# Optimization experiments

Measured on AMD Instinct MI355X. Metric: run time of the kernel, lower is better.

The kernel has to match this reference:

```python
import jax, jax.numpy as jnp
import numpy as np
import math

BS, S, DIM, H = 2, 2048, 1024, 16
DH = DIM // H


def setup_inputs() -> dict:
    key = jax.random.key(0)
    ks = jax.random.split(key, 11)
    std = 1.0 / math.sqrt(DIM)
    inp = {
        "query": jax.random.normal(ks[0], (BS, S, DIM), jnp.float32),
        "key_": jax.random.normal(ks[1], (BS, S, DIM), jnp.float32),
        "value": jax.random.normal(ks[2], (BS, S, DIM), jnp.float32),
        "mask": jnp.ones((BS, S), jnp.int32),
        "q_w": jax.random.normal(ks[3], (DIM, DIM), jnp.float32) * std,
        "q_b": jnp.zeros((DIM,), jnp.float32),
        "k_w": jax.random.normal(ks[4], (DIM, DIM), jnp.float32) * std,
        "k_b": jnp.zeros((DIM,), jnp.float32),
        "v_w": jax.random.normal(ks[5], (DIM, DIM), jnp.float32) * std,
        "v_b": jnp.zeros((DIM,), jnp.float32),
        "o_w": jax.random.normal(ks[6], (DIM, DIM), jnp.float32) * std,
        "o_b": jnp.zeros((DIM,), jnp.float32),
    }
    return inp


def _shape(x):
    # (bs, s, dim) -> (bs, h, s, dh)
    return x.reshape(BS, -1, H, DH).transpose(0, 2, 1, 3)


def reference(query, key_, value, mask, q_w, q_b, k_w, k_b, v_w, v_b, o_w, o_b):
    # linear projections (torch Linear: x @ W.T + b)
    q = _shape(query @ q_w.T + q_b) / math.sqrt(DH)
    k = _shape(key_ @ k_w.T + k_b)
    v = _shape(value @ v_w.T + v_b)
    # scores: (bs, h, s, s)
    scores = jnp.einsum("bhqd,bhkd->bhqk", q, k)
    pad = (mask == 0)[:, None, None, :]  # (bs,1,1,k_len)
    scores = jnp.where(pad, -jnp.inf, scores)
    weights = jax.nn.softmax(scores, axis=-1)
    context = jnp.einsum("bhqk,bhkd->bhqd", weights, v)
    context = context.transpose(0, 2, 1, 3).reshape(BS, -1, DIM)
    return context @ o_w.T + o_b
```

## Files before the change

### kernel.cpp

```cpp
#include <hip/hip_runtime.h>
#include <hip/hip_bf16.h>

#define BSZ 2
#define SEQ 2048
#define DIMN 1024
#define NH 16
#define DH 64
#define LOG2E 1.4426950408889634f

typedef unsigned short ushort_t;
typedef __attribute__((ext_vector_type(8))) short short8;
typedef __attribute__((ext_vector_type(4))) float float4v;

__device__ __forceinline__ ushort_t f2bf(float f) {
    union { float f; unsigned int u; } c; c.f = f;
    return (ushort_t)((c.u + 0x8000u) >> 16);
}
__device__ __forceinline__ unsigned int pkbf(float a, float b) {
    __hip_bfloat162 h = __float22bfloat162_rn(make_float2(a, b));
    unsigned int u; __builtin_memcpy(&u, &h, 4); return u;
}
__device__ __forceinline__ unsigned int pkbf_asm(float a, float b) {
    unsigned int d;
    asm("v_cvt_pk_bf16_f32 %0, %1, %2" : "=v"(d) : "v"(a), "v"(b));
    return d;
}
__device__ __forceinline__ float exp2_raw(float x) {
    float d; asm("v_exp_f32 %0, %1" : "=v"(d) : "v"(x)); return d;
}
__device__ __forceinline__ float max3f(float a, float b, float c) {
    float d; asm("v_max3_f32 %0, %1, %2, %3" : "=v"(d) : "v"(a), "v"(b), "v"(c)); return d;
}
__device__ __forceinline__ void gld16(const ushort_t* g, ushort_t* l) {
    __builtin_amdgcn_global_load_lds(
        (const __attribute__((address_space(1))) unsigned int*)g,
        (__attribute__((address_space(3))) unsigned int*)l, 16, 0, 0);
}

__global__ __launch_bounds__(256) void cvt_w4(
    const float* __restrict__ w0, const float* __restrict__ w1,
    const float* __restrict__ w2, const float* __restrict__ w3,
    ushort_t* __restrict__ o0, ushort_t* __restrict__ o1,
    ushort_t* __restrict__ o2, ushort_t* __restrict__ o3)
{
    const float* s; ushort_t* d;
    switch (blockIdx.y) {
        case 0: s = w0; d = o0; break;
        case 1: s = w1; d = o1; break;
        case 2: s = w2; d = o2; break;
        default: s = w3; d = o3; break;
    }
    int i = (blockIdx.x * 256 + threadIdx.x) * 4;
    float4v v = *(const float4v*)(s + i);
    uint2 o; o.x = pkbf(v[0], v[1]); o.y = pkbf(v[2], v[3]);
    *(uint2*)(d + i) = o;
}

__global__ __launch_bounds__(256) void gemm_qkv_hyb(
    const float* __restrict__ xq, const float* __restrict__ xk, const float* __restrict__ xv,
    const ushort_t* __restrict__ Wq, const ushort_t* __restrict__ Wk, const ushort_t* __restrict__ Wv,
    const float* __restrict__ qb, const float* __restrict__ kb, const float* __restrict__ vb,
    ushort_t* __restrict__ Qp, ushort_t* __restrict__ Kp, ushort_t* __restrict__ VpT)
{
    __shared__ __align__(16) ushort_t As[128 * 64];
    __shared__ __align__(16) ushort_t Bs[128 * 64];
    const int tid  = threadIdx.x;
    const int lane = tid & 63;
    const int w    = tid >> 6;
    const int wm   = w >> 1, wn = w & 1;
    const int quad = lane >> 4;
    const int l16  = lane & 15;
    const int sw   = l16 & 7;

    const int orig = blockIdx.x;
    const int swz  = (orig & 7) * 96 + (orig >> 3);
    const int bx   = swz % 24;
    const int by   = swz / 24;

    const int mBase = by * 128;
    const int nGlob = bx * 128;
    const int z     = nGlob >> 10;
    const int nBase = nGlob & 1023;
    const float*    A    = (z == 0) ? xq : (z == 1) ? xk : xv;
    const ushort_t* W    = (z == 0) ? Wq : (z == 1) ? Wk : Wv;
    const float*    bias = (z == 0) ? qb : (z == 1) ? kb : vb;

    const int srow = tid >> 3;
    const int sc   = tid & 7;

    float4v acc[4][4];
    const float4v z4 = {0.f, 0.f, 0.f, 0.f};
#pragma unroll
    for (int i = 0; i < 4; ++i)
#pragma unroll
        for (int j = 0; j < 4; ++j) acc[i][j] = z4;

    for (int k0 = 0; k0 < 1024; k0 += 64) {
#pragma unroll
        for (int itq = 0; itq < 4; ++itq) {
            int row = itq * 32 + srow;
            int colsw = (sc ^ (row & 7)) * 8;
            gld16(W + (size_t)(nBase + row) * 1024 + k0 + colsw, &Bs[(itq * 32 + w * 8) * 64]);
        }
#pragma unroll
        for (int it = 0; it < 4; ++it) {
            int c = it * 256 + tid, row = c >> 3, col8 = c & 7;
            const float* g = A + (size_t)(mBase + row) * 1024 + k0 + col8 * 8;
            float4v a0 = *(const float4v*)g;
            float4v a1 = *(const float4v*)(g + 4);
            uint4 ua;
            ua.x = pkbf(a0[0], a0[1]); ua.y = pkbf(a0[2], a0[3]);
            ua.z = pkbf(a1[0], a1[1]); ua.w = pkbf(a1[2], a1[3]);
            *(uint4*)&As[row * 64 + ((col8 ^ (row & 7)) * 8)] = ua;
        }
        __syncthreads();

#pragma unroll
        for (int ksub = 0; ksub < 2; ++ksub) {
            short8 af[4], bf[4];
#pragma unroll
            for (int mt = 0; mt < 4; ++mt)
                af[mt] = *(const short8*)&As[(wm * 64 + mt * 16 + l16) * 64 + ((ksub * 4 + quad) ^ sw) * 8];
#pragma unroll
            for (int nt = 0; nt < 4; ++nt)
                bf[nt] = *(const short8*)&Bs[(wn * 64 + nt * 16 + l16) * 64 + ((ksub * 4 + quad) ^ sw) * 8];
#pragma unroll
            for (int mt = 0; mt < 4; ++mt)
#pragma unroll
                for (int nt = 0; nt < 4; ++nt)
                    acc[mt][nt] = __builtin_amdgcn_mfma_f32_16x16x32_bf16(af[mt], bf[nt], acc[mt][nt], 0, 0, 0);
        }
        __syncthreads();
    }

    const float scale = (z == 0) ? 0.125f * LOG2E : 1.0f;
    if (z < 2) {
        ushort_t* C = (z == 0) ? Qp : Kp;
#pragma unroll
        for (int mt = 0; mt < 4; ++mt)
#pragma unroll
            for (int nt = 0; nt < 4; ++nt) {
                int colg = nBase + wn * 64 + nt * 16 + l16;
                float bv = bias[colg];
#pragma unroll
                for (int r = 0; r < 4; ++r) {
                    int rowg = mBase + wm * 64 + mt * 16 + quad * 4 + r;
                    C[(size_t)rowg * 1024 + colg] = f2bf((acc[mt][nt][r] + bv) * scale);
                }
            }
    } else {
#pragma unroll
        for (int mt = 0; mt < 4; ++mt)
#pragma unroll
            for (int nt = 0; nt < 4; ++nt) {
                int n = nBase + wn * 64 + nt * 16 + l16;
                int hh = n >> 6, d = n & 63;
                float bv = bias[n];
                int rowg = mBase + wm * 64 + mt * 16 + quad * 4;
                int b = rowg >> 11, s = rowg & 2047;
                uint2 pk;
                pk.x = pkbf(acc[mt][nt][0] + bv, acc[mt][nt][1] + bv);
                pk.y = pkbf(acc[mt][nt][2] + bv, acc[mt][nt][3] + bv);
                *(uint2*)&VpT[(((size_t)(b * 16 + hh) * 64 + d) << 11) + s] = pk;
            }
    }
}

__global__ __launch_bounds__(256) void gemm_o(
    const ushort_t* __restrict__ A, const ushort_t* __restrict__ W,
    const float* __restrict__ bias, float* __restrict__ C)
{
    __shared__ __align__(16) ushort_t As[128 * 64];
    __shared__ __align__(16) ushort_t Bs[64 * 64];
    const int tid  = threadIdx.x;
    const int lane = tid & 63;
    const int w    = tid >> 6;
    const int wm   = w & 1, wn = w >> 1;
    const int quad = lane >> 4;
    const int l16  = lane & 15;
    const int sw   = l16 & 7;

    const int orig = blockIdx.x;
    const int swz  = (orig & 7) * 64 + (orig >> 3);
    const int nBase = (swz & 15) * 64;
    const int mBase = (swz >> 4) * 128;

    const int srow = tid >> 3;
    const int sc   = tid & 7;

    float4v acc[4][2];
    const float4v z4 = {0.f, 0.f, 0.f, 0.f};
#pragma unroll
    for (int mt = 0; mt < 4; ++mt)
#pragma unroll
        for (int nt = 0; nt < 2; ++nt) acc[mt][nt] = z4;

    for (int k0 = 0; k0 < 1024; k0 += 64) {
#pragma unroll
        for (int itq = 0; itq < 4; ++itq) {
            int row = itq * 32 + srow;
            gld16(A + (size_t)(mBase + row) * 1024 + k0 + ((sc ^ (row & 7)) * 8),
                  &As[(itq * 32 + w * 8) * 64]);
        }
#pragma unroll
        for (int itq = 0; itq < 2; ++itq) {
            int row = itq * 32 + srow;
            gld16(W + (size_t)(nBase + row) * 1024 + k0 + ((sc ^ (row & 7)) * 8),
                  &Bs[(itq * 32 + w * 8) * 64]);
        }
        __syncthreads();

#pragma unroll
        for (int ksub = 0; ksub < 2; ++ksub) {
            short8 af[4], bf[2];
#pragma unroll
            for (int mt = 0; mt < 4; ++mt)
                af[mt] = *(const short8*)&As[(wm * 64 + mt * 16 + l16) * 64 + ((ksub * 4 + quad) ^ sw) * 8];
#pragma unroll
            for (int nt = 0; nt < 2; ++nt)
                bf[nt] = *(const short8*)&Bs[(wn * 32 + nt * 16 + l16) * 64 + ((ksub * 4 + quad) ^ sw) * 8];
#pragma unroll
            for (int mt = 0; mt < 4; ++mt)
#pragma unroll
                for (int nt = 0; nt < 2; ++nt)
                    acc[mt][nt] = __builtin_amdgcn_mfma_f32_16x16x32_bf16(af[mt], bf[nt], acc[mt][nt], 0, 0, 0);
        }
        __syncthreads();
    }

#pragma unroll
    for (int mt = 0; mt < 4; ++mt)
#pragma unroll
        for (int nt = 0; nt < 2; ++nt) {
            int colg = nBase + wn * 32 + nt * 16 + l16;
            float bv = bias[colg];
#pragma unroll
            for (int r = 0; r < 4; ++r) {
                int rowg = mBase + wm * 64 + mt * 16 + quad * 4 + r;
                C[(size_t)rowg * 1024 + colg] = acc[mt][nt][r] + bv;
            }
        }
}

__global__ __launch_bounds__(512) void attn_kernel(
    const ushort_t* __restrict__ Qp, const ushort_t* __restrict__ Kp,
    const ushort_t* __restrict__ VpT, const int* __restrict__ mask,
    ushort_t* __restrict__ Cp)
{
    __shared__ __align__(16) ushort_t Ps[2][128 * 64];
    __shared__ __align__(16) ushort_t Ks[2][64 * 64];
    __shared__ __align__(16) ushort_t Vt[3][64 * 64];
    __shared__ int s_mok[8];

    const int tid  = threadIdx.x;
    const int lane = tid & 63;
    const int w    = tid >> 6;
    const int quad = lane >> 4;
    const int l16  = lane & 15;
    const int sw   = l16 & 7;
    const int b    = blockIdx.x >> 4;
    const int h    = blockIdx.x & 15;
    const int q0   = blockIdx.y * 128;

    const int srow = tid >> 3;
    const int sc   = tid & 7;
    const int gsc  = (sc ^ (srow & 7)) * 8;
    const ushort_t* Vbase = VpT + ((size_t)(b * 16 + h) * 64) * 2048;
    const ushort_t* Kbase = Kp + (size_t)b * SEQ * DIMN + h * DH;
    const ushort_t* Qbase = Qp + (size_t)(b * SEQ + q0) * DIMN + h * DH;

    {
        int m0 = mask[b * SEQ + tid];
        int m1 = mask[b * SEQ + 512 + tid];
        int m2 = mask[b * SEQ + 1024 + tid];
        int m3 = mask[b * SEQ + 1536 + tid];
        int ok = __all((m0 != 0) & (m1 != 0) & (m2 != 0) & (m3 != 0));
        if (lane == 0) s_mok[w] = ok;
    }

#pragma unroll
    for (int it2 = 0; it2 < 2; ++it2) {
        int row = it2 * 64 + srow;
        gld16(Qbase + (size_t)row * DIMN + ((sc ^ (row & 7)) * 8),
              &Ps[0][(it2 * 64 + w * 8) * 64]);
    }
    gld16(Kbase + (size_t)srow * DIMN + gsc, &Ks[0][w * 512]);
    gld16(Vbase + (size_t)srow * 2048 + gsc, &Vt[0][w * 512]);
    __syncthreads();

    const int mall = s_mok[0] & s_mok[1] & s_mok[2] & s_mok[3]
                   & s_mok[4] & s_mok[5] & s_mok[6] & s_mok[7];

    short8 bq[2];
#pragma unroll
    for (int ks = 0; ks < 2; ++ks)
        bq[ks] = *(const short8*)&Ps[0][(w * 16 + l16) * 64 + ((4 * ks + quad) ^ sw) * 8];

    const float4v z4 = {0.f, 0.f, 0.f, 0.f};
    float4v Oacc[4];
#pragma unroll
    for (int vt = 0; vt < 4; ++vt) Oacc[vt] = z4;
    float4v Lacc = z4;
    float mrow = 0.0f;
    float4v mneg4 = z4;

    short8 ones;
#pragma unroll
    for (int j = 0; j < 8; ++j) ones[j] = (short)0x3F80;

    const int NT = SEQ / 64;
    const int prow = (w * 16 + l16) * 64;

    {
        gld16(Kbase + (size_t)(64 + srow) * DIMN + gsc, &Ks[1][w * 512]);
        gld16(Vbase + (size_t)srow * 2048 + 64 + gsc, &Vt[1][w * 512]);

        float4v Sv[4];
        __builtin_amdgcn_s_setprio(1);
#pragma unroll
        for (int kt = 0; kt < 4; ++kt) {
            short8 ak = *(const short8*)&Ks[0][(kt * 16 + l16) * 64 + (quad ^ sw) * 8];
            Sv[kt] = __builtin_amdgcn_mfma_f32_16x16x32_bf16(ak, bq[0], mneg4, 0, 0, 0);
        }
#pragma unroll
        for (int kt = 0; kt < 4; ++kt) {
            short8 ak = *(const short8*)&Ks[0][(kt * 16 + l16) * 64 + ((4 + quad) ^ sw) * 8];
            Sv[kt] = __builtin_amdgcn_mfma_f32_16x16x32_bf16(ak, bq[1], Sv[kt], 0, 0, 0);
        }
        __builtin_amdgcn_s_setprio(0);

        if (!mall) {
#pragma unroll
            for (int kt = 0; kt < 4; ++kt) {
                int4 mv = *(const int4*)(mask + b * SEQ + kt * 16 + quad * 4);
#pragma unroll
                for (int r = 0; r < 4; ++r) {
                    int m = (r == 0) ? mv.x : (r == 1) ? mv.y : (r == 2) ? mv.z : mv.w;
                    Sv[kt][r] += (m == 0) ? -1e30f : 0.0f;
                }
            }
        }

        float a0 = max3f(Sv[0][0], Sv[0][1], Sv[0][2]);
        float a1 = max3f(Sv[0][3], Sv[1][0], Sv[1][1]);
        float a2 = max3f(Sv[1][2], Sv[1][3], Sv[2][0]);
        float a3 = max3f(Sv[2][1], Sv[2][2], Sv[2][3]);
        float a4 = max3f(Sv[3][0], Sv[3][1], Sv[3][2]);
        float b0 = max3f(a0, a1, Sv[3][3]);
        float b1 = max3f(a2, a3, a4);
        float mx = fmaxf(b0, b1);
        mx = fmaxf(mx, __shfl_xor(mx, 16));
        mx = fmaxf(mx, __shfl_xor(mx, 32));
        if (!__all(mx <= 8.0f)) {
            float d = fmaxf(mx, 0.0f);
            float alpha = exp2_raw(-d);
            mrow += d;
#pragma unroll
            for (int vt = 0; vt < 4; ++vt) Oacc[vt] *= alpha;
            Lacc *= alpha;
#pragma unroll
            for (int kt = 0; kt < 4; ++kt)
#pragma unroll
                for (int r = 0; r < 4; ++r) Sv[kt][r] -= d;
            mneg4[0] = -mrow; mneg4[1] = -mrow; mneg4[2] = -mrow; mneg4[3] = -mrow;
        }
#pragma unroll
        for (int kt = 0; kt < 4; ++kt)
#pragma unroll
            for (int r = 0; r < 4; ++r) Sv[kt][r] = exp2_raw(Sv[kt][r]);

#pragma unroll
        for (int kt = 0; kt < 4; ++kt) {
            uint2 pk;
            pk.x = pkbf_asm(Sv[kt][0], Sv[kt][1]);
            pk.y = pkbf_asm(Sv[kt][2], Sv[kt][3]);
            int chunk = (2 * kt + (quad >> 1)) ^ sw;
            *(uint2*)&Ps[0][prow + chunk * 8 + (quad & 1) * 4] = pk;
        }
        __syncthreads();
    }

    ushort_t* vRd  = Vt[0];
    ushort_t* vCur = Vt[1];
    ushort_t* vWr  = Vt[2];

#pragma unroll 2
    for (int t = 1; t < NT; ++t) {
        const int kt0 = t * 64;

        if (t + 1 < NT) {
            gld16(Kbase + (size_t)(kt0 + 64 + srow) * DIMN + gsc, &Ks[(t + 1) & 1][w * 512]);
            gld16(Vbase + (size_t)srow * 2048 + kt0 + 64 + gsc, vWr + w * 512);
        }

        float4v Sv[4];
        __builtin_amdgcn_s_setprio(1);
#pragma unroll
        for (int kt = 0; kt < 4; ++kt) {
            short8 ak = *(const short8*)&Ks[t & 1][(kt * 16 + l16) * 64 + (quad ^ sw) * 8];
            Sv[kt] = __builtin_amdgcn_mfma_f32_16x16x32_bf16(ak, bq[0], mneg4, 0, 0, 0);
        }
#pragma unroll
        for (int kt = 0; kt < 4; ++kt) {
            short8 ak = *(const short8*)&Ks[t & 1][(kt * 16 + l16) * 64 + ((4 + quad) ^ sw) * 8];
            Sv[kt] = __builtin_amdgcn_mfma_f32_16x16x32_bf16(ak, bq[1], Sv[kt], 0, 0, 0);
        }
#pragma unroll
        for (int ks = 0; ks < 2; ++ks) {
            short8 bp = *(const short8*)&Ps[(t - 1) & 1][prow + ((4 * ks + quad) ^ sw) * 8];
            Lacc = __builtin_amdgcn_mfma_f32_16x16x32_bf16(ones, bp, Lacc, 0, 0, 0);
#pragma unroll
            for (int vt = 0; vt < 4; ++vt) {
                short8 av = *(const short8*)(vRd + (vt * 16 + l16) * 64 + ((4 * ks + quad) ^ sw) * 8);
                Oacc[vt] = __builtin_amdgcn_mfma_f32_16x16x32_bf16(av, bp, Oacc[vt], 0, 0, 0);
            }
        }
        __builtin_amdgcn_s_setprio(0);

        if (!mall) {
#pragma unroll
            for (int kt = 0; kt < 4; ++kt) {
                int4 mv = *(const int4*)(mask + b * SEQ + kt0 + kt * 16 + quad * 4);
#pragma unroll
                for (int r = 0; r < 4; ++r) {
                    int m = (r == 0) ? mv.x : (r == 1) ? mv.y : (r == 2) ? mv.z : mv.w;
                    Sv[kt][r] += (m == 0) ? -1e30f : 0.0f;
                }
            }
        }

        float a0 = max3f(Sv[0][0], Sv[0][1], Sv[0][2]);
        float a1 = max3f(Sv[0][3], Sv[1][0], Sv[1][1]);
        float a2 = max3f(Sv[1][2], Sv[1][3], Sv[2][0]);
        float a3 = max3f(Sv[2][1], Sv[2][2], Sv[2][3]);
        float a4 = max3f(Sv[3][0], Sv[3][1], Sv[3][2]);
        float b0 = max3f(a0, a1, Sv[3][3]);
        float b1 = max3f(a2, a3, a4);
        float mx = fmaxf(b0, b1);
        mx = fmaxf(mx, __shfl_xor(mx, 16));
        mx = fmaxf(mx, __shfl_xor(mx, 32));
        if (!__all(mx <= 8.0f)) {
            float d = fmaxf(mx, 0.0f);
            float alpha = exp2_raw(-d);
            mrow += d;
#pragma unroll
            for (int vt = 0; vt < 4; ++vt) Oacc[vt] *= alpha;
            Lacc *= alpha;
#pragma unroll
            for (int kt = 0; kt < 4; ++kt)
#pragma unroll
                for (int r = 0; r < 4; ++r) Sv[kt][r] -= d;
            mneg4[0] = -mrow; mneg4[1] = -mrow; mneg4[2] = -mrow; mneg4[3] = -mrow;
        }
#pragma unroll
        for (int kt = 0; kt < 4; ++kt)
#pragma unroll
            for (int r = 0; r < 4; ++r) Sv[kt][r] = exp2_raw(Sv[kt][r]);

#pragma unroll
        for (int kt = 0; kt < 4; ++kt) {
            uint2 pk;
            pk.x = pkbf_asm(Sv[kt][0], Sv[kt][1]);
            pk.y = pkbf_asm(Sv[kt][2], Sv[kt][3]);
            int chunk = (2 * kt + (quad >> 1)) ^ sw;
            *(uint2*)&Ps[t & 1][prow + chunk * 8 + (quad & 1) * 4] = pk;
        }

        __syncthreads();

        ushort_t* tmp = vRd; vRd = vCur; vCur = vWr; vWr = tmp;
    }

#pragma unroll
    for (int ks = 0; ks < 2; ++ks) {
        short8 bp = *(const short8*)&Ps[(NT - 1) & 1][prow + ((4 * ks + quad) ^ sw) * 8];
        Lacc = __builtin_amdgcn_mfma_f32_16x16x32_bf16(ones, bp, Lacc, 0, 0, 0);
#pragma unroll
        for (int vt = 0; vt < 4; ++vt) {
            short8 av = *(const short8*)(vRd + (vt * 16 + l16) * 64 + ((4 * ks + quad) ^ sw) * 8);
            Oacc[vt] = __builtin_amdgcn_mfma_f32_16x16x32_bf16(av, bp, Oacc[vt], 0, 0, 0);
        }
    }

    float inv = 1.0f / Lacc[0];
    int row = q0 + w * 16 + l16;
#pragma unroll
    for (int vt = 0; vt < 4; ++vt) {
        uint2 pk;
        pk.x = pkbf_asm(Oacc[vt][0] * inv, Oacc[vt][1] * inv);
        pk.y = pkbf_asm(Oacc[vt][2] * inv, Oacc[vt][3] * inv);
        *(uint2*)&Cp[(size_t)(b * SEQ + row) * DIMN + h * DH + vt * 16 + quad * 4] = pk;
    }
}

extern "C" void kernel_launch(void* const* d_in, const int* in_sizes, int n_in,
                              void* d_out, int out_size, void* d_ws, size_t ws_size,
                              hipStream_t stream) {
    const float* x_q = (const float*)d_in[0];
    const float* x_k = (const float*)d_in[1];
    const float* x_v = (const float*)d_in[2];
    const int*   msk = (const int*)d_in[3];
    const float* q_w = (const float*)d_in[4];
    const float* q_b = (const float*)d_in[5];
    const float* k_w = (const float*)d_in[6];
    const float* k_b = (const float*)d_in[7];
    const float* v_w = (const float*)d_in[8];
    const float* v_b = (const float*)d_in[9];
    const float* o_w = (const float*)d_in[10];
    const float* o_b = (const float*)d_in[11];
    float* out = (float*)d_out;

    const size_t NEL = (size_t)BSZ * SEQ * DIMN;
    const size_t WEL = (size_t)DIMN * DIMN;
    ushort_t* Qp  = (ushort_t*)d_ws;
    ushort_t* Kp  = Qp + NEL;
    ushort_t* VpT = Kp + NEL;
    ushort_t* Wq  = VpT + NEL;
    ushort_t* Wk  = Wq + WEL;
    ushort_t* Wv  = Wk + WEL;
    ushort_t* Wo  = Wv + WEL;
    ushort_t* Cp  = Qp;

    cvt_w4<<<dim3(WEL / 1024, 4), 256, 0, stream>>>(q_w, k_w, v_w, o_w, Wq, Wk, Wv, Wo);
    gemm_qkv_hyb<<<dim3(768), 256, 0, stream>>>(x_q, x_k, x_v, Wq, Wk, Wv,
                                                q_b, k_b, v_b, Qp, Kp, VpT);
    attn_kernel<<<dim3(BSZ * NH, SEQ / 128), 512, 0, stream>>>(Qp, Kp, VpT, msk, Cp);
    gemm_o<<<dim3(512), 256, 0, stream>>>(Cp, Wo, o_b, out);
}
```

Baseline: 231.0 us.

## Pre-convert activations to bf16 and enlarge output-projection GEMM tiles

Folds the conversion of the three fp32 input activations into the weight-conversion kernel, so the QKV GEMM can load both operands as bf16 through direct global-to-LDS loads. This removes the per-tile fp32 load, convert and LDS-store path from the GEMM inner loop. In exchange it adds a full extra write and read of the bf16 activations (about 25 MB of extra traffic) plus workspace. The output GEMM also moves from 128x64 to 128x128 tiles, which halves the grid to 256 blocks and gives more reuse per block but may lower occupancy.

```diff
diff --git a/kernel.cpp b/kernel.cpp
--- a/kernel.cpp
+++ b/kernel.cpp
@@ -37,27 +37,45 @@
         (__attribute__((address_space(3))) unsigned int*)l, 16, 0, 0);
 }
 
-__global__ __launch_bounds__(256) void cvt_w4(
+__global__ __launch_bounds__(256) void cvt_all(
     const float* __restrict__ w0, const float* __restrict__ w1,
     const float* __restrict__ w2, const float* __restrict__ w3,
+    const float* __restrict__ x0, const float* __restrict__ x1,
+    const float* __restrict__ x2,
     ushort_t* __restrict__ o0, ushort_t* __restrict__ o1,
-    ushort_t* __restrict__ o2, ushort_t* __restrict__ o3)
+    ushort_t* __restrict__ o2, ushort_t* __restrict__ o3,
+    ushort_t* __restrict__ xb)
 {
-    const float* s; ushort_t* d;
-    switch (blockIdx.y) {
-        case 0: s = w0; d = o0; break;
-        case 1: s = w1; d = o1; break;
-        case 2: s = w2; d = o2; break;
-        default: s = w3; d = o3; break;
-    }
-    int i = (blockIdx.x * 256 + threadIdx.x) * 4;
-    float4v v = *(const float4v*)(s + i);
-    uint2 o; o.x = pkbf(v[0], v[1]); o.y = pkbf(v[2], v[3]);
-    *(uint2*)(d + i) = o;
-}
-
-__global__ __launch_bounds__(256) void gemm_qkv_hyb(
-    const float* __restrict__ xq, const float* __restrict__ xk, const float* __restrict__ xv,
+    const int y = blockIdx.y;
+    if (y < 4) {
+        const float* s; ushort_t* d;
+        switch (y) {
+            case 0: s = w0; d = o0; break;
+            case 1: s = w1; d = o1; break;
+            case 2: s = w2; d = o2; break;
+            default: s = w3; d = o3; break;
+        }
+        int i = (blockIdx.x * 256 + threadIdx.x) * 4;
+        float4v v = *(const float4v*)(s + i);
+        uint2 o; o.x = pkbf(v[0], v[1]); o.y = pkbf(v[2], v[3]);
+        *(uint2*)(d + i) = o;
+    } else {
+        const int m = y - 4;
+        const float* s = (m == 0) ? x0 : (m == 1) ? x1 : x2;
+        ushort_t* d = xb + (size_t)m * (BSZ * SEQ * DIMN);
+        size_t base = (size_t)blockIdx.x * 4096;
+#pragma unroll
+        for (int j = 0; j < 4; ++j) {
+            size_t i = base + j * 1024 + threadIdx.x * 4;
+            float4v v = *(const float4v*)(s + i);
+            uint2 o; o.x = pkbf(v[0], v[1]); o.y = pkbf(v[2], v[3]);
+            *(uint2*)(d + i) = o;
+        }
+    }
+}
+
+__global__ __launch_bounds__(256) void gemm_qkv_fast(
+    const ushort_t* __restrict__ Xb,
     const ushort_t* __restrict__ Wq, const ushort_t* __restrict__ Wk, const ushort_t* __restrict__ Wv,
     const float* __restrict__ qb, const float* __restrict__ kb, const float* __restrict__ vb,
     ushort_t* __restrict__ Qp, ushort_t* __restrict__ Kp, ushort_t* __restrict__ VpT)
@@ -81,7 +99,7 @@
     const int nGlob = bx * 128;
     const int z     = nGlob >> 10;
     const int nBase = nGlob & 1023;
-    const float*    A    = (z == 0) ? xq : (z == 1) ? xk : xv;
+    const ushort_t* A    = Xb + (size_t)z * (BSZ * SEQ * DIMN);
     const ushort_t* W    = (z == 0) ? Wq : (z == 1) ? Wk : Wv;
     const float*    bias = (z == 0) ? qb : (z == 1) ? kb : vb;
 
@@ -100,18 +118,8 @@
         for (int itq = 0; itq < 4; ++itq) {
             int row = itq * 32 + srow;
             int colsw = (sc ^ (row & 7)) * 8;
+            gld16(A + (size_t)(mBase + row) * 1024 + k0 + colsw, &As[(itq * 32 + w * 8) * 64]);
             gld16(W + (size_t)(nBase + row) * 1024 + k0 + colsw, &Bs[(itq * 32 + w * 8) * 64]);
-        }
-#pragma unroll
-        for (int it = 0; it < 4; ++it) {
-            int c = it * 256 + tid, row = c >> 3, col8 = c & 7;
-            const float* g = A + (size_t)(mBase + row) * 1024 + k0 + col8 * 8;
-            float4v a0 = *(const float4v*)g;
-            float4v a1 = *(const float4v*)(g + 4);
-            uint4 ua;
-            ua.x = pkbf(a0[0], a0[1]); ua.y = pkbf(a0[2], a0[3]);
-            ua.z = pkbf(a1[0], a1[1]); ua.w = pkbf(a1[2], a1[3]);
-            *(uint4*)&As[row * 64 + ((col8 ^ (row & 7)) * 8)] = ua;
         }
         __syncthreads();
 
@@ -171,58 +179,53 @@
     const float* __restrict__ bias, float* __restrict__ C)
 {
     __shared__ __align__(16) ushort_t As[128 * 64];
-    __shared__ __align__(16) ushort_t Bs[64 * 64];
+    __shared__ __align__(16) ushort_t Bs[128 * 64];
     const int tid  = threadIdx.x;
     const int lane = tid & 63;
     const int w    = tid >> 6;
-    const int wm   = w & 1, wn = w >> 1;
+    const int wm   = w >> 1, wn = w & 1;
     const int quad = lane >> 4;
     const int l16  = lane & 15;
     const int sw   = l16 & 7;
 
     const int orig = blockIdx.x;
-    const int swz  = (orig & 7) * 64 + (orig >> 3);
-    const int nBase = (swz & 15) * 64;
-    const int mBase = (swz >> 4) * 128;
+    const int swz  = (orig & 7) * 32 + (orig >> 3);
+    const int nBase = (swz & 7) * 128;
+    const int mBase = (swz >> 3) * 128;
 
     const int srow = tid >> 3;
     const int sc   = tid & 7;
 
-    float4v acc[4][2];
+    float4v acc[4][4];
     const float4v z4 = {0.f, 0.f, 0.f, 0.f};
 #pragma unroll
-    for (int mt = 0; mt < 4; ++mt)
-#pragma unroll
-        for (int nt = 0; nt < 2; ++nt) acc[mt][nt] = z4;
+    for (int i = 0; i < 4; ++i)
+#pragma unroll
+        for (int j = 0; j < 4; ++j) acc[i][j] = z4;
 
     for (int k0 = 0; k0 < 1024; k0 += 64) {
 #pragma unroll
         for (int itq = 0; itq < 4; ++itq) {
             int row = itq * 32 + srow;
-            gld16(A + (size_t)(mBase + row) * 1024 + k0 + ((sc ^ (row & 7)) * 8),
-                  &As[(itq * 32 + w * 8) * 64]);
-        }
-#pragma unroll
-        for (int itq = 0; itq < 2; ++itq) {
-            int row = itq * 32 + srow;
-            gld16(W + (size_t)(nBase + row) * 1024 + k0 + ((sc ^ (row & 7)) * 8),
-                  &Bs[(itq * 32 + w * 8) * 64]);
+            int colsw = (sc ^ (row & 7)) * 8;
+            gld16(A + (size_t)(mBase + row) * 1024 + k0 + colsw, &As[(itq * 32 + w * 8) * 64]);
+            gld16(W + (size_t)(nBase + row) * 1024 + k0 + colsw, &Bs[(itq * 32 + w * 8) * 64]);
         }
         __syncthreads();
 
 #pragma unroll
         for (int ksub = 0; ksub < 2; ++ksub) {
-            short8 af[4], bf[2];
+            short8 af[4], bf[4];
 #pragma unroll
             for (int mt = 0; mt < 4; ++mt)
                 af[mt] = *(const short8*)&As[(wm * 64 + mt * 16 + l16) * 64 + ((ksub * 4 + quad) ^ sw) * 8];
 #pragma unroll
-            for (int nt = 0; nt < 2; ++nt)
-                bf[nt] = *(const short8*)&Bs[(wn * 32 + nt * 16 + l16) * 64 + ((ksub * 4 + quad) ^ sw) * 8];
+            for (int nt = 0; nt < 4; ++nt)
+                bf[nt] = *(const short8*)&Bs[(wn * 64 + nt * 16 + l16) * 64 + ((ksub * 4 + quad) ^ sw) * 8];
 #pragma unroll
             for (int mt = 0; mt < 4; ++mt)
 #pragma unroll
-                for (int nt = 0; nt < 2; ++nt)
+                for (int nt = 0; nt < 4; ++nt)
                     acc[mt][nt] = __builtin_amdgcn_mfma_f32_16x16x32_bf16(af[mt], bf[nt], acc[mt][nt], 0, 0, 0);
         }
         __syncthreads();
@@ -231,8 +234,8 @@
 #pragma unroll
     for (int mt = 0; mt < 4; ++mt)
 #pragma unroll
-        for (int nt = 0; nt < 2; ++nt) {
-            int colg = nBase + wn * 32 + nt * 16 + l16;
+        for (int nt = 0; nt < 4; ++nt) {
+            int colg = nBase + wn * 64 + nt * 16 + l16;
             float bv = bias[colg];
 #pragma unroll
             for (int r = 0; r < 4; ++r) {
@@ -519,11 +522,13 @@
     ushort_t* Wk  = Wq + WEL;
     ushort_t* Wv  = Wk + WEL;
     ushort_t* Wo  = Wv + WEL;
+    ushort_t* Xb  = Wo + WEL;
     ushort_t* Cp  = Qp;
 
-    cvt_w4<<<dim3(WEL / 1024, 4), 256, 0, stream>>>(q_w, k_w, v_w, o_w, Wq, Wk, Wv, Wo);
-    gemm_qkv_hyb<<<dim3(768), 256, 0, stream>>>(x_q, x_k, x_v, Wq, Wk, Wv,
-                                                q_b, k_b, v_b, Qp, Kp, VpT);
+    cvt_all<<<dim3(1024, 7), 256, 0, stream>>>(q_w, k_w, v_w, o_w, x_q, x_k, x_v,
+                                               Wq, Wk, Wv, Wo, Xb);
+    gemm_qkv_fast<<<dim3(768), 256, 0, stream>>>(Xb, Wq, Wk, Wv,
+                                                 q_b, k_b, v_b, Qp, Kp, VpT);
     attn_kernel<<<dim3(BSZ * NH, SEQ / 128), 512, 0, stream>>>(Qp, Kp, VpT, msk, Cp);
-    gemm_o<<<dim3(512), 256, 0, stream>>>(Cp, Wo, o_b, out);
-}
+    gemm_o<<<dim3(256), 256, 0, stream>>>(Cp, Wo, o_b, out);
+}
```

After: 231.3 us. No clear change (+0.1%).
